# Optimization experiments

Measured on AMD Instinct MI355X. Metric: run time of the kernel, lower is better.

## Reference

```python
import jax, jax.numpy as jnp
import numpy as np

B, T, H = 1024, 256, 128

def _gru(x, Wx, Wh, b):
    # Keras GRU (reset_after=True), gate order z, r, h. x: [B,T,D], b: [2,3H]
    xp = x @ Wx + b[0]                      # [B,T,3H]
    h0 = jnp.zeros((x.shape[0], Wh.shape[0]), x.dtype)
    def step(h, xt):
        hp = h @ Wh + b[1]
        xz, xr, xh = jnp.split(xt, 3, axis=-1)
        hz, hr, hn = jnp.split(hp, 3, axis=-1)
        z = jax.nn.sigmoid(xz + hz)
        r = jax.nn.sigmoid(xr + hr)
        hh = jnp.tanh(xh + r * hn)
        return z * h + (1.0 - z) * hh, None
    h, _ = jax.lax.scan(step, h0, jnp.swapaxes(xp, 0, 1))
    return h                                 # [B,H]

def setup_inputs() -> dict:
    key = jax.random.key(0)
    ks = jax.random.split(key, 32)
    def gp(k, shape, scale=0.05):
        return (jax.random.normal(k, shape, dtype=jnp.float32) * scale)
    inp = {
        "spatial": jax.random.normal(ks[0], (B, T, 2), dtype=jnp.float32),
        "hour_idx": jax.random.randint(ks[1], (B, T), 0, 24, dtype=jnp.int32),
        "week_idx": jax.random.randint(ks[2], (B, T), 0, 7, dtype=jnp.int32),
        "E_time": gp(ks[3], (24, H)),
        "E_week": gp(ks[4], (7, H)),
        # spatial GRU (input dim 2)
        "Ws_x": gp(ks[5], (2, 3 * H)), "Ws_h": gp(ks[6], (H, 3 * H)), "bs": gp(ks[7], (2, 3 * H)),
        # hour temporal GRU (input dim 128)
        "Wh_x": gp(ks[8], (H, 3 * H)), "Wh_h": gp(ks[9], (H, 3 * H)), "bh": gp(ks[10], (2, 3 * H)),
        # week temporal GRU (input dim 128)
        "Ww_x": gp(ks[11], (H, 3 * H)), "Ww_h": gp(ks[12], (H, 3 * H)), "bw": gp(ks[13], (2, 3 * H)),
        # attention Dense(3) over the channel axis of size 3
        "Wa": gp(ks[14], (3, 3)), "ba": gp(ks[15], (3,)),
        # MLP
        "W1": gp(ks[16], (H, 1024)), "b1": gp(ks[17], (1024,)),
        "W2": gp(ks[18], (1024, 512)), "b2": gp(ks[19], (512,)),
        "W3": gp(ks[20], (512, 256)), "b3": gp(ks[21], (256,)),
        "W4": gp(ks[22], (256, H)), "b4": gp(ks[23], (H,)),
        "Wo": gp(ks[24], (H, 1)), "bo": gp(ks[25], (1,)),
    }
    return inp

def reference(spatial, hour_idx, week_idx, E_time, E_week,
              Ws_x, Ws_h, bs, Wh_x, Wh_h, bh, Ww_x, Ww_h, bw,
              Wa, ba, W1, b1, W2, b2, W3, b3, W4, b4, Wo, bo):
    te = E_time[hour_idx]                    # [B,T,128] gather
    we = E_week[week_idx]                    # [B,T,128] gather
    fs = _gru(spatial, Ws_x, Ws_h, bs)       # [B,128]
    fh = _gru(te, Wh_x, Wh_h, bh)            # [B,128]
    fw = _gru(we, Ww_x, Ww_h, bw)            # [B,128]
    allf = jnp.stack([fs, fh, fw], axis=-1)  # [B,128,3]
    scores = jax.nn.softmax(jax.nn.relu(allf @ Wa + ba), axis=-1)
    sf = jnp.sum(allf * scores, axis=-1)     # [B,128] attention-fused features
    x = jax.nn.relu(sf @ W1 + b1)
    x = jax.nn.relu(x @ W2 + b2)
    x = jax.nn.relu(x @ W3 + b3)
    x = jax.nn.relu(x @ W4 + b4)
    out = (x + sf) @ Wo + bo                 # residual then Dense(1)
    return out[:, 0]                         # [B]
```

## Files before the change

### kernel.cpp

```cpp
#include <hip/hip_runtime.h>
#include <hip/hip_bf16.h>

typedef __attribute__((ext_vector_type(8))) short short8;
typedef __attribute__((ext_vector_type(4))) float f32x4;
typedef __attribute__((ext_vector_type(2))) float f32x2;
typedef __attribute__((ext_vector_type(2))) unsigned u32x2;

#define LOG2E  1.44269504088896340736f
#define NLOG2E (-1.44269504088896340736f)
#define TLOG2E (2.88539008177792681472f)

#define HES 168

__device__ __forceinline__ unsigned short f2bf(float f) {
  unsigned u = __builtin_bit_cast(unsigned, f);
  u += 0x7fffu + ((u >> 16) & 1u);
  return (unsigned short)(u >> 16);
}

__global__ __launch_bounds__(256) void ptab_kernel(
    const float* __restrict__ E_time, const float* __restrict__ E_week,
    const float* __restrict__ Wh_x, const float* __restrict__ bh,
    const float* __restrict__ Ww_x, const float* __restrict__ bw,
    float* __restrict__ Ptime, float* __restrict__ Pweek)
{
  const int b = blockIdx.x;
  for (int c = threadIdx.x; c < 384; c += 256) {
    if (b < 24) {
      float acc = bh[c];
      for (int d = 0; d < 128; ++d)
        acc = fmaf(E_time[b * 128 + d], Wh_x[d * 384 + c], acc);
      Ptime[b * 384 + c] = acc;
    } else {
      const int r = b - 24;
      float acc = bw[c];
      for (int d = 0; d < 128; ++d)
        acc = fmaf(E_week[r * 128 + d], Ww_x[d * 384 + c], acc);
      Pweek[r * 384 + c] = acc;
    }
  }
}

__global__ __launch_bounds__(512, 2) void gru_kernel(
    const float* __restrict__ spatial,
    const int* __restrict__ hour_idx,
    const int* __restrict__ week_idx,
    const float* __restrict__ Ws_x,
    const float* __restrict__ Ws_h, const float* __restrict__ bs,
    const float* __restrict__ Wh_h, const float* __restrict__ bh,
    const float* __restrict__ Ww_h, const float* __restrict__ bw,
    const float* __restrict__ Ptime, const float* __restrict__ Pweek,
    const float* __restrict__ W1, const float* __restrict__ W2,
    const float* __restrict__ W3, const float* __restrict__ W4,
    unsigned short* __restrict__ Wt,
    float* __restrict__ fs, float* __restrict__ fh, float* __restrict__ fw)
{
  __shared__ __align__(16) unsigned char smem_u[64 * 65 * 4];
  unsigned short (*hx)[16 * HES] = (unsigned short (*)[16 * HES])smem_u;

  const int tid = threadIdx.x;

  if (blockIdx.x >= 192) {
    float (*ttile)[65] = (float (*)[65])smem_u;
    const int tx = tid & 63, ty = tid >> 6;
    for (int t0 = blockIdx.x - 192; t0 < 200; t0 += 64) {
      int tb = t0;
      const float* src; unsigned short* dst; int K, N, tk, tn;
      if (tb < 32)       { src = W1; dst = Wt;          K = 128;  N = 1024; tk = tb >> 4; tn = tb & 15; }
      else if (tb < 160) { tb -= 32;  src = W2; dst = Wt + 131072; K = 1024; N = 512;  tk = tb >> 3; tn = tb & 7; }
      else if (tb < 192) { tb -= 160; src = W3; dst = Wt + 655360; K = 512;  N = 256;  tk = tb >> 2; tn = tb & 3; }
      else               { tb -= 192; src = W4; dst = Wt + 786432; K = 256;  N = 128;  tk = tb >> 1; tn = tb & 1; }
      const int k0 = tk * 64, n0 = tn * 64;
      #pragma unroll
      for (int i = 0; i < 8; ++i)
        ttile[ty * 8 + i][tx] = src[(k0 + ty * 8 + i) * N + n0 + tx];
      __syncthreads();
      #pragma unroll
      for (int i = 0; i < 8; ++i)
        dst[(n0 + ty * 8 + i) * K + k0 + tx] = f2bf(ttile[tx][ty * 8 + i]);
      __syncthreads();
    }
    return;
  }

  const int lane = tid & 63;
  const int wv   = tid >> 6;
  const int ar   = lane & 15;
  const int akg  = lane >> 4;
  const int gid  = blockIdx.x;
  const int gru  = gid >> 6;
  const int row0 = (gid & 63) * 16;

  const float* __restrict__ Wh   = (gru == 0) ? Ws_h : (gru == 1) ? Wh_h : Ww_h;
  const float* __restrict__ bvec = (gru == 0) ? bs   : (gru == 1) ? bh   : bw;
  float* __restrict__ fout       = (gru == 0) ? fs   : (gru == 1) ? fh   : fw;
  const float* __restrict__ Ptab = (gru == 1) ? Ptime : Pweek;
  const int* __restrict__ idxg   = (gru == 1) ? hour_idx : week_idx;
  const int NR = (gru == 1) ? 24 : 7;

  const int j  = wv * 16 + ar;
  const int c4 = wv * 16 + akg * 4;

  short8 wf[15];
  #pragma unroll
  for (int g = 0; g < 2; ++g) {
    #pragma unroll
    for (int ks = 0; ks < 5; ++ks) {
      short8 f;
      #pragma unroll
      for (int q = 0; q < 8; ++q) {
        const int k = ks * 32 + akg * 8 + q;
        float v;
        if (k < 128) v = Wh[k * 384 + g * 128 + j];
        else {
          const int p = k - 128;
          if (gru == 0) v = (p == 0) ? Ws_x[g * 128 + j]
                          : (p == 1) ? Ws_x[384 + g * 128 + j] : 0.f;
          else          v = (p < NR) ? Ptab[p * 384 + g * 128 + j] : 0.f;
        }
        f[q] = (short)f2bf(v * NLOG2E);
      }
      wf[g * 5 + ks] = f;
    }
  }
  #pragma unroll
  for (int ks = 0; ks < 4; ++ks) {
    short8 f;
    #pragma unroll
    for (int q = 0; q < 8; ++q) {
      const int k = ks * 32 + akg * 8 + q;
      f[q] = (short)f2bf(Wh[k * 384 + 256 + j] * TLOG2E);
    }
    wf[10 + ks] = f;
  }
  {
    short8 f;
    #pragma unroll
    for (int q = 0; q < 8; ++q) {
      const int p = akg * 8 + q;
      float v;
      if (gru == 0) v = (p == 0) ? Ws_x[256 + j]
                      : (p == 1) ? Ws_x[384 + 256 + j] : 0.f;
      else          v = (p < NR) ? Ptab[p * 384 + 256 + j] : 0.f;
      f[q] = (short)f2bf(v * TLOG2E);
    }
    wf[14] = f;
  }

  f32x4 bzv, brv, bnhv, bnxv;
  {
    const f32x4 z1 = *(const f32x4*)&bvec[384 + c4];
    const f32x4 r1 = *(const f32x4*)&bvec[384 + 128 + c4];
    const f32x4 n1 = *(const f32x4*)&bvec[384 + 256 + c4];
    if (gru == 0) {
      const f32x4 z0 = *(const f32x4*)&bvec[c4];
      const f32x4 r0 = *(const f32x4*)&bvec[128 + c4];
      const f32x4 n0 = *(const f32x4*)&bvec[256 + c4];
      bzv = (z1 + z0) * NLOG2E; brv = (r1 + r0) * NLOG2E;
      bnhv = n1 * TLOG2E;       bnxv = n0 * TLOG2E;
    } else {
      bzv = z1 * NLOG2E; brv = r1 * NLOG2E;
      bnhv = n1 * TLOG2E; bnxv = f32x4{0.f, 0.f, 0.f, 0.f};
    }
  }

  for (int e = tid; e < 2 * 16 * HES; e += 512) ((unsigned short*)hx)[e] = 0;
  __syncthreads();

  const bool mt  = (tid & 31) == 0;
  const int mrow = tid >> 5;
  int ix_prev = 0, ix_cur = 0;
  if (mt) {
    if (gru == 0) {
      const f32x2 s = *(const f32x2*)&spatial[(row0 + mrow) * 512];
      unsigned pk;
      asm("v_cvt_pk_bf16_f32 %0, %1, %2" : "=v"(pk) : "v"(s.x), "v"(s.y));
      *(unsigned*)&hx[0][mrow * HES + 128] = pk;
    } else {
      ix_cur = idxg[(row0 + mrow) * 256];
      hx[0][mrow * HES + 128 + ix_cur] = 0x3F80;
    }
  }
  __syncthreads();

  float hst[4] = {0.f, 0.f, 0.f, 0.f};

  for (int t = 0; t < 256; ++t) {
    const unsigned short* __restrict__ hb = hx[t & 1];
    unsigned short* __restrict__ ho       = hx[(t + 1) & 1];

    short8 b[5];
    #pragma unroll
    for (int ks = 0; ks < 5; ++ks)
      b[ks] = *(const short8*)&hb[ar * HES + ks * 32 + akg * 8];

    f32x2 msp = {0.f, 0.f};
    int ix_next = 0;
    const bool mact = mt && (t + 1 < 256);
    if (mact) {
      if (gru == 0) msp = *(const f32x2*)&spatial[(row0 + mrow) * 512 + 2 * (t + 1)];
      else          ix_next = idxg[(row0 + mrow) * 256 + t + 1];
    }

    f32x4 az  = bzv;
    f32x4 arr = brv;
    f32x4 anh = bnhv;
    f32x4 anx = bnxv;
    #pragma unroll
    for (int ks = 0; ks < 4; ++ks) {
      az  = __builtin_amdgcn_mfma_f32_16x16x32_bf16(wf[ks],      b[ks], az,  0, 0, 0);
      arr = __builtin_amdgcn_mfma_f32_16x16x32_bf16(wf[5 + ks],  b[ks], arr, 0, 0, 0);
      anh = __builtin_amdgcn_mfma_f32_16x16x32_bf16(wf[10 + ks], b[ks], anh, 0, 0, 0);
    }
    az  = __builtin_amdgcn_mfma_f32_16x16x32_bf16(wf[4],  b[4], az,  0, 0, 0);
    arr = __builtin_amdgcn_mfma_f32_16x16x32_bf16(wf[9],  b[4], arr, 0, 0, 0);
    anx = __builtin_amdgcn_mfma_f32_16x16x32_bf16(wf[14], b[4], anx, 0, 0, 0);

    if (mact) {
      if (gru == 0) {
        unsigned pk;
        asm("v_cvt_pk_bf16_f32 %0, %1, %2" : "=v"(pk) : "v"(msp.x), "v"(msp.y));
        *(unsigned*)&ho[mrow * HES + 128] = pk;
      } else {
        if (t >= 1) ho[mrow * HES + 128 + ix_prev] = 0;
        ho[mrow * HES + 128 + ix_next] = 0x3F80;
        ix_prev = ix_cur; ix_cur = ix_next;
      }
    }

    float pz[4], pr[4];
    #pragma unroll
    for (int q = 0; q < 4; ++q) {
      pz[q] = 1.f + __builtin_amdgcn_exp2f(az[q]);
      pr[q] = 1.f + __builtin_amdgcn_exp2f(arr[q]);
    }
    float zg[4], rg[4];
    #pragma unroll
    for (int p = 0; p < 4; p += 2) {
      const float A0 = pz[p] * pr[p];
      const float A1 = pz[p + 1] * pr[p + 1];
      const float inv = __builtin_amdgcn_rcpf(A0 * A1);
      const float t1 = A1 * inv, t0 = A0 * inv;
      zg[p]     = pr[p] * t1;     rg[p]     = pz[p] * t1;
      zg[p + 1] = pr[p + 1] * t0; rg[p + 1] = pz[p + 1] * t0;
    }
    float ph[4];
    #pragma unroll
    for (int q = 0; q < 4; ++q)
      ph[q] = 1.f + __builtin_amdgcn_exp2f(fmaf(rg[q], anh[q], anx[q]));
    float hn4[4];
    #pragma unroll
    for (int p = 0; p < 4; p += 2) {
      const float inv = __builtin_amdgcn_rcpf(ph[p] * ph[p + 1]);
      const float hh0 = fmaf(-2.f, ph[p + 1] * inv, 1.f);
      const float hh1 = fmaf(-2.f, ph[p] * inv, 1.f);
      hn4[p]     = fmaf(zg[p],     hst[p]     - hh0, hh0);
      hn4[p + 1] = fmaf(zg[p + 1], hst[p + 1] - hh1, hh1);
      hst[p] = hn4[p]; hst[p + 1] = hn4[p + 1];
    }

    unsigned p01, p23;
    asm("v_cvt_pk_bf16_f32 %0, %1, %2" : "=v"(p01) : "v"(hn4[0]), "v"(hn4[1]));
    asm("v_cvt_pk_bf16_f32 %0, %1, %2" : "=v"(p23) : "v"(hn4[2]), "v"(hn4[3]));
    *(u32x2*)&ho[ar * HES + c4] = u32x2{p01, p23};

    __syncthreads();
  }

  {
    const f32x4 v = {hst[0], hst[1], hst[2], hst[3]};
    *(f32x4*)&fout[(row0 + ar) * 128 + c4] = v;
  }
}

template<int K, int N>
__device__ __forceinline__ void mlp_layer(
    const unsigned short* __restrict__ xin, unsigned short* __restrict__ xout,
    const unsigned short* __restrict__ Wt, const float* __restrict__ bias,
    int lane, int wv, float* __restrict__ foutF)
{
  constexpr int NT = N / 128;
  const int ar  = lane & 15;
  const int akg = lane >> 4;
  f32x4 acc[NT];
  #pragma unroll
  for (int nt = 0; nt < NT; ++nt) acc[nt] = f32x4{0.f, 0.f, 0.f, 0.f};
  for (int ks = 0; ks < K / 32; ++ks) {
    const short8 a = *(const short8*)&xin[ar * 1032 + ks * 32 + akg * 8];
    #pragma unroll
    for (int nt = 0; nt < NT; ++nt) {
      const int n = wv * (N / 8) + nt * 16 + ar;
      const short8 b = *(const short8*)&Wt[n * K + ks * 32 + akg * 8];
      acc[nt] = __builtin_amdgcn_mfma_f32_16x16x32_bf16(a, b, acc[nt], 0, 0, 0);
    }
  }
  const int rbase = akg * 4;
  #pragma unroll
  for (int nt = 0; nt < NT; ++nt) {
    const int n = wv * (N / 8) + nt * 16 + ar;
    const float bv = bias[n];
    #pragma unroll
    for (int q = 0; q < 4; ++q) {
      float v = acc[nt][q] + bv;
      v = fmaxf(v, 0.f);
      xout[(rbase + q) * 1032 + n] = f2bf(v);
      if (foutF) foutF[(rbase + q) * 128 + n] = v;
    }
  }
}

__global__ __launch_bounds__(512) void attn_mlp_kernel(
    const float* __restrict__ fs, const float* __restrict__ fh, const float* __restrict__ fw,
    const float* __restrict__ Wa, const float* __restrict__ ba,
    const unsigned short* __restrict__ Wt,
    const float* __restrict__ b1, const float* __restrict__ b2,
    const float* __restrict__ b3, const float* __restrict__ b4,
    const float* __restrict__ Wo, const float* __restrict__ bo,
    float* __restrict__ out)
{
  __shared__ __align__(16) unsigned short xa[16 * 1032];
  __shared__ __align__(16) unsigned short xb[16 * 1032];
  __shared__ __align__(16) float sf_l[16 * 128];
  __shared__ __align__(16) float x4f[16 * 128];

  const int tid  = threadIdx.x;
  const int lane = tid & 63;
  const int wv   = tid >> 6;
  const int row0 = blockIdx.x * 16;

  {
    const int i  = tid >> 5;
    const int j0 = (tid & 31) * 4;
    float wa[9], bav[3];
    #pragma unroll
    for (int q = 0; q < 9; ++q) wa[q] = Wa[q];
    #pragma unroll
    for (int q = 0; q < 3; ++q) bav[q] = ba[q];
    const int base = (row0 + i) * 128 + j0;
    const f32x4 a = *(const f32x4*)&fs[base];
    const f32x4 b = *(const f32x4*)&fh[base];
    const f32x4 c = *(const f32x4*)&fw[base];
    #pragma unroll
    for (int q = 0; q < 4; ++q) {
      const float f0 = a[q], f1 = b[q], f2 = c[q];
      float s0 = f0 * wa[0] + f1 * wa[3] + f2 * wa[6] + bav[0];
      float s1 = f0 * wa[1] + f1 * wa[4] + f2 * wa[7] + bav[1];
      float s2 = f0 * wa[2] + f1 * wa[5] + f2 * wa[8] + bav[2];
      s0 = fmaxf(s0, 0.f); s1 = fmaxf(s1, 0.f); s2 = fmaxf(s2, 0.f);
      const float m  = fmaxf(s0, fmaxf(s1, s2));
      const float e0 = __builtin_amdgcn_exp2f((s0 - m) * LOG2E);
      const float e1 = __builtin_amdgcn_exp2f((s1 - m) * LOG2E);
      const float e2 = __builtin_amdgcn_exp2f((s2 - m) * LOG2E);
      const float inv = __builtin_amdgcn_rcpf(e0 + e1 + e2);
      const float sf  = (f0 * e0 + f1 * e1 + f2 * e2) * inv;
      const int jj = j0 + q;
      sf_l[i * 128 + jj] = sf;
      xa[i * 1032 + jj]  = f2bf(sf);
    }
  }
  __syncthreads();

  mlp_layer<128, 1024>(xa, xb, Wt,          b1, lane, wv, nullptr);
  __syncthreads();
  mlp_layer<1024, 512>(xb, xa, Wt + 131072, b2, lane, wv, nullptr);
  __syncthreads();
  mlp_layer<512,  256>(xa, xb, Wt + 655360, b3, lane, wv, nullptr);
  __syncthreads();
  mlp_layer<256,  128>(xb, xa, Wt + 786432, b4, lane, wv, x4f);
  __syncthreads();

  const int row = tid >> 5;
  const int p   = tid & 31;
  float part = 0.f;
  #pragma unroll
  for (int q = 0; q < 4; ++q) {
    const int jj = p + q * 32;
    part += (x4f[row * 128 + jj] + sf_l[row * 128 + jj]) * Wo[jj];
  }
  #pragma unroll
  for (int off = 16; off > 0; off >>= 1)
    part += __shfl_xor(part, off, 32);
  if (p == 0) out[row0 + row] = part + bo[0];
}

extern "C" void kernel_launch(void* const* d_in, const int* in_sizes, int n_in,
                              void* d_out, int out_size, void* d_ws, size_t ws_size,
                              hipStream_t stream) {
  const float* spatial  = (const float*)d_in[0];
  const int*   hour_idx = (const int*)d_in[1];
  const int*   week_idx = (const int*)d_in[2];
  const float* E_time   = (const float*)d_in[3];
  const float* E_week   = (const float*)d_in[4];
  const float* Ws_x = (const float*)d_in[5];
  const float* Ws_h = (const float*)d_in[6];
  const float* bs   = (const float*)d_in[7];
  const float* Wh_x = (const float*)d_in[8];
  const float* Wh_h = (const float*)d_in[9];
  const float* bh   = (const float*)d_in[10];
  const float* Ww_x = (const float*)d_in[11];
  const float* Ww_h = (const float*)d_in[12];
  const float* bw   = (const float*)d_in[13];
  const float* Wa   = (const float*)d_in[14];
  const float* ba   = (const float*)d_in[15];
  const float* W1   = (const float*)d_in[16];
  const float* b1   = (const float*)d_in[17];
  const float* W2   = (const float*)d_in[18];
  const float* b2   = (const float*)d_in[19];
  const float* W3   = (const float*)d_in[20];
  const float* b3   = (const float*)d_in[21];
  const float* W4   = (const float*)d_in[22];
  const float* b4   = (const float*)d_in[23];
  const float* Wo   = (const float*)d_in[24];
  const float* bo   = (const float*)d_in[25];
  float* out = (float*)d_out;

  float* ws    = (float*)d_ws;
  float* Ptime = ws;
  float* Pweek = Ptime + 9216;
  float* fsb   = Pweek + 2688;
  float* fhb   = fsb + 131072;
  float* fwb   = fhb + 131072;
  unsigned short* Wt = (unsigned short*)(fwb + 131072);

  ptab_kernel<<<31, 256, 0, stream>>>(E_time, E_week, Wh_x, bh, Ww_x, bw, Ptime, Pweek);
  gru_kernel<<<256, 512, 0, stream>>>(spatial, hour_idx, week_idx, Ws_x,
      Ws_h, bs, Wh_h, bh, Ww_h, bw, Ptime, Pweek,
      W1, W2, W3, W4, Wt, fsb, fhb, fwb);
  attn_mlp_kernel<<<64, 512, 0, stream>>>(fsb, fhb, fwb, Wa, ba, Wt,
      b1, b2, b3, b4, Wo, bo, out);
}
```

Before: 230.8 us.

## Fuse embedding projection table into GRU kernel and halve MLP rows per block

Removes the separate ptab kernel launch. Each temporal GRU block now computes the embedding-times-Wx projection table into shared memory itself, which drops one launch and its dependency barrier but repeats the small table computation in every block. Separately, the attention+MLP kernel now processes 8 rows per block over 128 blocks instead of 16 rows over 64 blocks, with the upper half of the MFMA input tile zero-padded, to raise parallelism at the cost of wasted MFMA work and more weight reads.

```diff
diff --git a/kernel.cpp b/kernel.cpp
--- a/kernel.cpp
+++ b/kernel.cpp
@@ -18,45 +18,25 @@
   return (unsigned short)(u >> 16);
 }
 
-__global__ __launch_bounds__(256) void ptab_kernel(
-    const float* __restrict__ E_time, const float* __restrict__ E_week,
-    const float* __restrict__ Wh_x, const float* __restrict__ bh,
-    const float* __restrict__ Ww_x, const float* __restrict__ bw,
-    float* __restrict__ Ptime, float* __restrict__ Pweek)
-{
-  const int b = blockIdx.x;
-  for (int c = threadIdx.x; c < 384; c += 256) {
-    if (b < 24) {
-      float acc = bh[c];
-      for (int d = 0; d < 128; ++d)
-        acc = fmaf(E_time[b * 128 + d], Wh_x[d * 384 + c], acc);
-      Ptime[b * 384 + c] = acc;
-    } else {
-      const int r = b - 24;
-      float acc = bw[c];
-      for (int d = 0; d < 128; ++d)
-        acc = fmaf(E_week[r * 128 + d], Ww_x[d * 384 + c], acc);
-      Pweek[r * 384 + c] = acc;
-    }
-  }
-}
-
 __global__ __launch_bounds__(512, 2) void gru_kernel(
     const float* __restrict__ spatial,
     const int* __restrict__ hour_idx,
     const int* __restrict__ week_idx,
+    const float* __restrict__ E_time, const float* __restrict__ E_week,
     const float* __restrict__ Ws_x,
     const float* __restrict__ Ws_h, const float* __restrict__ bs,
+    const float* __restrict__ Wh_x,
     const float* __restrict__ Wh_h, const float* __restrict__ bh,
+    const float* __restrict__ Ww_x,
     const float* __restrict__ Ww_h, const float* __restrict__ bw,
-    const float* __restrict__ Ptime, const float* __restrict__ Pweek,
     const float* __restrict__ W1, const float* __restrict__ W2,
     const float* __restrict__ W3, const float* __restrict__ W4,
     unsigned short* __restrict__ Wt,
     float* __restrict__ fs, float* __restrict__ fh, float* __restrict__ fw)
 {
-  __shared__ __align__(16) unsigned char smem_u[64 * 65 * 4];
+  __shared__ __align__(16) unsigned char smem_u[48 * 1024];
   unsigned short (*hx)[16 * HES] = (unsigned short (*)[16 * HES])smem_u;
+  float* P_lds = (float*)(smem_u + 2 * 16 * HES * 2);
 
   const int tid = threadIdx.x;
 
@@ -94,9 +74,22 @@
   const float* __restrict__ Wh   = (gru == 0) ? Ws_h : (gru == 1) ? Wh_h : Ww_h;
   const float* __restrict__ bvec = (gru == 0) ? bs   : (gru == 1) ? bh   : bw;
   float* __restrict__ fout       = (gru == 0) ? fs   : (gru == 1) ? fh   : fw;
-  const float* __restrict__ Ptab = (gru == 1) ? Ptime : Pweek;
   const int* __restrict__ idxg   = (gru == 1) ? hour_idx : week_idx;
   const int NR = (gru == 1) ? 24 : 7;
+
+  if (gru != 0) {
+    const float* __restrict__ E  = (gru == 1) ? E_time : E_week;
+    const float* __restrict__ Wx = (gru == 1) ? Wh_x : Ww_x;
+    for (int e = tid; e < NR * 384; e += 512) {
+      const int p = e / 384, c = e - p * 384;
+      float acc = bvec[c];
+      #pragma unroll 8
+      for (int d = 0; d < 128; ++d)
+        acc = fmaf(E[p * 128 + d], Wx[d * 384 + c], acc);
+      P_lds[p * 384 + c] = acc;
+    }
+  }
+  __syncthreads();
 
   const int j  = wv * 16 + ar;
   const int c4 = wv * 16 + akg * 4;
@@ -116,7 +109,7 @@
           const int p = k - 128;
           if (gru == 0) v = (p == 0) ? Ws_x[g * 128 + j]
                           : (p == 1) ? Ws_x[384 + g * 128 + j] : 0.f;
-          else          v = (p < NR) ? Ptab[p * 384 + g * 128 + j] : 0.f;
+          else          v = (p < NR) ? P_lds[p * 384 + g * 128 + j] : 0.f;
         }
         f[q] = (short)f2bf(v * NLOG2E);
       }
@@ -141,7 +134,7 @@
       float v;
       if (gru == 0) v = (p == 0) ? Ws_x[256 + j]
                       : (p == 1) ? Ws_x[384 + 256 + j] : 0.f;
-      else          v = (p < NR) ? Ptab[p * 384 + 256 + j] : 0.f;
+      else          v = (p < NR) ? P_lds[p * 384 + 256 + j] : 0.f;
       f[q] = (short)f2bf(v * TLOG2E);
     }
     wf[14] = f;
@@ -326,22 +319,24 @@
   const int tid  = threadIdx.x;
   const int lane = tid & 63;
   const int wv   = tid >> 6;
-  const int row0 = blockIdx.x * 16;
+  const int row0 = blockIdx.x * 8;
+
+  for (int e = tid; e < 8 * 1032; e += 512) xa[8 * 1032 + e] = 0;
 
   {
-    const int i  = tid >> 5;
-    const int j0 = (tid & 31) * 4;
+    const int i  = tid >> 6;
+    const int p2 = (tid & 63) * 2;
     float wa[9], bav[3];
     #pragma unroll
     for (int q = 0; q < 9; ++q) wa[q] = Wa[q];
     #pragma unroll
     for (int q = 0; q < 3; ++q) bav[q] = ba[q];
-    const int base = (row0 + i) * 128 + j0;
-    const f32x4 a = *(const f32x4*)&fs[base];
-    const f32x4 b = *(const f32x4*)&fh[base];
-    const f32x4 c = *(const f32x4*)&fw[base];
-    #pragma unroll
-    for (int q = 0; q < 4; ++q) {
+    const int base = (row0 + i) * 128 + p2;
+    const f32x2 a = *(const f32x2*)&fs[base];
+    const f32x2 b = *(const f32x2*)&fh[base];
+    const f32x2 c = *(const f32x2*)&fw[base];
+    #pragma unroll
+    for (int q = 0; q < 2; ++q) {
       const float f0 = a[q], f1 = b[q], f2 = c[q];
       float s0 = f0 * wa[0] + f1 * wa[3] + f2 * wa[6] + bav[0];
       float s1 = f0 * wa[1] + f1 * wa[4] + f2 * wa[7] + bav[1];
@@ -353,7 +348,7 @@
       const float e2 = __builtin_amdgcn_exp2f((s2 - m) * LOG2E);
       const float inv = __builtin_amdgcn_rcpf(e0 + e1 + e2);
       const float sf  = (f0 * e0 + f1 * e1 + f2 * e2) * inv;
-      const int jj = j0 + q;
+      const int jj = p2 + q;
       sf_l[i * 128 + jj] = sf;
       xa[i * 1032 + jj]  = f2bf(sf);
     }
@@ -369,17 +364,17 @@
   mlp_layer<256,  128>(xb, xa, Wt + 786432, b4, lane, wv, x4f);
   __syncthreads();
 
-  const int row = tid >> 5;
-  const int p   = tid & 31;
+  const int row = tid >> 6;
+  const int p   = tid & 63;
   float part = 0.f;
   #pragma unroll
-  for (int q = 0; q < 4; ++q) {
-    const int jj = p + q * 32;
+  for (int q = 0; q < 2; ++q) {
+    const int jj = p + q * 64;
     part += (x4f[row * 128 + jj] + sf_l[row * 128 + jj]) * Wo[jj];
   }
   #pragma unroll
-  for (int off = 16; off > 0; off >>= 1)
-    part += __shfl_xor(part, off, 32);
+  for (int off = 32; off > 0; off >>= 1)
+    part += __shfl_xor(part, off, 64);
   if (p == 0) out[row0 + row] = part + bo[0];
 }
 
@@ -415,17 +410,14 @@
   float* out = (float*)d_out;
 
   float* ws    = (float*)d_ws;
-  float* Ptime = ws;
-  float* Pweek = Ptime + 9216;
-  float* fsb   = Pweek + 2688;
+  float* fsb   = ws;
   float* fhb   = fsb + 131072;
   float* fwb   = fhb + 131072;
   unsigned short* Wt = (unsigned short*)(fwb + 131072);
 
-  ptab_kernel<<<31, 256, 0, stream>>>(E_time, E_week, Wh_x, bh, Ww_x, bw, Ptime, Pweek);
-  gru_kernel<<<256, 512, 0, stream>>>(spatial, hour_idx, week_idx, Ws_x,
-      Ws_h, bs, Wh_h, bh, Ww_h, bw, Ptime, Pweek,
+  gru_kernel<<<256, 512, 0, stream>>>(spatial, hour_idx, week_idx,
+      E_time, E_week, Ws_x, Ws_h, bs, Wh_x, Wh_h, bh, Ww_x, Ww_h, bw,
       W1, W2, W3, W4, Wt, fsb, fhb, fwb);
-  attn_mlp_kernel<<<64, 512, 0, stream>>>(fsb, fhb, fwb, Wa, ba, Wt,
+  attn_mlp_kernel<<<128, 512, 0, stream>>>(fsb, fhb, fwb, Wa, ba, Wt,
       b1, b2, b3, b4, Wo, bo, out);
 }
```

New measurement: 287.2 us. 1.24x slower.
